# Performance work log

Measured on AMD Instinct MI355X. Metric: run time of the kernel, lower is better.

## Reference

```python
import math
import jax, jax.numpy as jnp
import numpy as np

EPS = 1e-5
KS = 8          # emb_ks == emb_hs
NH = 4          # attention heads
LOOKBACK = 5
NLAYERS = 4


def prelu(x, a):
    return jnp.where(x >= 0, x, a * x)


def ln_c(x, g, b):
    # LayerNormalization4D: stats over channel dim; note (std + eps) denominator
    mu = jnp.mean(x, 1, keepdims=True)
    var = jnp.mean((x - mu) ** 2, 1, keepdims=True)
    return (x - mu) / (jnp.sqrt(var + EPS) + EPS) * g[None, :, None, None] + b[None, :, None, None]


def ln_cf_head(x, g, b):
    # x: [H, B, E, T, F]; stats over (E, F); g, b: [H, E, F]
    mu = jnp.mean(x, (2, 4), keepdims=True)
    var = jnp.mean((x - mu) ** 2, (2, 4), keepdims=True)
    return (x - mu) / (jnp.sqrt(var + EPS) + EPS) * g[:, None, :, None, :] + b[:, None, :, None, :]


def ln_cf_proj(x, g, b):
    # x: [B, C, T, F]; stats over (C, F); g, b: [C, F]
    mu = jnp.mean(x, (1, 3), keepdims=True)
    var = jnp.mean((x - mu) ** 2, (1, 3), keepdims=True)
    return (x - mu) / (jnp.sqrt(var + EPS) + EPS) * g[None, :, None, :] + b[None, :, None, :]


def lstm(x, wih, whh, bih, bhh):
    # x: [N, T, I] -> hidden sequence [N, T, H]; PyTorch gate order i, f, g, o
    xp = jnp.einsum('nti,gi->ntg', x, wih) + bih + bhh
    H = whh.shape[1]
    N = x.shape[0]

    def step(carry, xt):
        h, c = carry
        gates = xt + h @ whh.T
        i, f, g, o = jnp.split(gates, 4, axis=-1)
        c = jax.nn.sigmoid(f) * c + jax.nn.sigmoid(i) * jnp.tanh(g)
        h = jax.nn.sigmoid(o) * jnp.tanh(c)
        return (h, c), h

    init = (jnp.zeros((N, H), x.dtype), jnp.zeros((N, H), x.dtype))
    _, hs = jax.lax.scan(step, init, jnp.swapaxes(xp, 0, 1))
    return jnp.swapaxes(hs, 0, 1)


def bilstm(x, wih, whh, bih, bhh):
    fwd = lstm(x, wih[0], whh[0], bih[0], bhh[0])
    bwd = lstm(x[:, ::-1], wih[1], whh[1], bih[1], bhh[1])[:, ::-1]
    return jnp.concatenate([fwd, bwd], -1)


def unfold1d(x):
    # non-overlapping unfold (ks == stride == KS): [N, C, L] -> [N, L//KS, C*KS]
    N, C, Lx = x.shape
    return x.reshape(N, C, Lx // KS, KS).transpose(0, 2, 1, 3).reshape(N, Lx // KS, C * KS)


def fold1d(h, w, b):
    # ConvTranspose1d with stride == kernel == KS; h: [N, Lp, D], w: [D, C, KS]
    y = jnp.einsum('nld,dck->nlck', h, w)
    N, Lp, C, K = y.shape
    return y.transpose(0, 2, 1, 3).reshape(N, C, Lp * K) + b[None, :, None]


def conv2d(x, w, b):
    y = jax.lax.conv_general_dilated(x, w, (1, 1), ((1, 1), (1, 1)),
                                     dimension_numbers=('NCHW', 'OIHW', 'NCHW'))
    return y + b[None, :, None, None]


def block(x, p):
    B, C, oT, oF = x.shape
    T = math.ceil((oT - KS) / KS) * KS + KS
    F = math.ceil((oF - KS) / KS) * KS + KS
    x = jnp.pad(x, ((0, 0), (0, 0), (0, T - oT), (0, F - oF)))
    input_ = x
    # intra (frequency) bidirectional LSTM
    z = ln_c(input_, p['intra_norm_g'], p['intra_norm_b'])
    z = z.transpose(0, 2, 1, 3).reshape(B * T, C, F)
    z = unfold1d(z)                                    # [B*T, F//KS, C*KS]
    h = bilstm(z, p['intra_wih'], p['intra_whh'], p['intra_bih'], p['intra_bhh'])
    z = fold1d(h, p['intra_lin_w'], p['intra_lin_b'])  # [B*T, C, F]
    intra = z.reshape(B, T, C, F).transpose(0, 2, 1, 3) + input_
    # inter (time) causal LSTM
    z = ln_c(intra, p['inter_norm_g'], p['inter_norm_b'])
    z = z.transpose(0, 3, 1, 2).reshape(B * F, C, T)
    z = unfold1d(z)                                    # [B*F, T//KS, C*KS]
    h = lstm(z, p['inter_wih'], p['inter_whh'], p['inter_bih'], p['inter_bhh'])
    z = fold1d(h, p['inter_lin_w'], p['inter_lin_b'])  # [B*F, C, T]
    inter = z.reshape(B, F, C, T).transpose(0, 2, 3, 1) + intra
    inter = inter[..., :oT, :oF]

    # per-head 1x1-conv QKV (batched over heads) + local causal attention
    def qkv(w, b, a, g, beta):
        y = jnp.einsum('bctf,hec->hbetf', inter, w) + b[:, None, :, None, None]
        y = prelu(y, a[:, None, None, None, None])
        return ln_cf_head(y, g, beta)

    Q = qkv(p['q_w'], p['q_b'], p['q_a'], p['q_g'], p['q_beta'])
    K = qkv(p['k_w'], p['k_b'], p['k_a'], p['k_g'], p['k_beta'])
    V = qkv(p['v_w'], p['v_b'], p['v_a'], p['v_g'], p['v_beta'])
    E = Q.shape[2]
    CV = V.shape[2]
    Qf = Q.transpose(0, 1, 3, 2, 4).reshape(NH, B, oT, E * oF)
    Kf = K.transpose(0, 1, 3, 2, 4).reshape(NH, B, oT, E * oF)
    Vf = V.transpose(0, 1, 3, 2, 4).reshape(NH, B, oT, CV * oF)
    attn = jnp.einsum('hbtd,hbsd->hbts', Qf, Kf) / jnp.sqrt(jnp.asarray(E * oF, Qf.dtype))
    t = jnp.arange(oT)
    d = t[:, None] - t[None, :]
    mask = (d >= 0) & (d <= LOOKBACK)      # causal with 5-frame lookback
    attn = jnp.where(mask, attn, -1e30)
    A = jax.nn.softmax(attn, axis=-1)
    O = jnp.einsum('hbts,hbsd->hbtd', A, Vf).reshape(NH, B, oT, CV, oF)
    O = O.transpose(1, 0, 3, 2, 4).reshape(B, NH * CV, oT, oF)
    y = jnp.einsum('bctf,dc->bdtf', O, p['proj_w']) + p['proj_b'][None, :, None, None]
    y = prelu(y, p['proj_a'])
    y = ln_cf_proj(y, p['proj_g'], p['proj_beta'])
    return y + inter


def _forward(x, conv_w, conv_b, gn_g, gn_b,
             intra_norm_g, intra_norm_b, intra_wih, intra_whh, intra_bih, intra_bhh,
             intra_lin_w, intra_lin_b,
             inter_norm_g, inter_norm_b, inter_wih, inter_whh, inter_bih, inter_bhh,
             inter_lin_w, inter_lin_b,
             q_w, q_b, q_a, q_g, q_beta,
             k_w, k_b, k_a, k_g, k_beta,
             v_w, v_b, v_a, v_g, v_beta,
             proj_w, proj_b, proj_a, proj_g, proj_beta,
             deconv_w, deconv_b):
    esti = conv2d(x, conv_w, conv_b)
    # GroupNorm(1, emb_dim): per-sample stats over (C, T, F), per-channel affine
    mu = jnp.mean(esti, (1, 2, 3), keepdims=True)
    var = jnp.mean((esti - mu) ** 2, (1, 2, 3), keepdims=True)
    esti = (esti - mu) / jnp.sqrt(var + EPS) * gn_g[None, :, None, None] + gn_b[None, :, None, None]
    stacked = dict(
        intra_norm_g=intra_norm_g, intra_norm_b=intra_norm_b,
        intra_wih=intra_wih, intra_whh=intra_whh, intra_bih=intra_bih, intra_bhh=intra_bhh,
        intra_lin_w=intra_lin_w, intra_lin_b=intra_lin_b,
        inter_norm_g=inter_norm_g, inter_norm_b=inter_norm_b,
        inter_wih=inter_wih, inter_whh=inter_whh, inter_bih=inter_bih, inter_bhh=inter_bhh,
        inter_lin_w=inter_lin_w, inter_lin_b=inter_lin_b,
        q_w=q_w, q_b=q_b, q_a=q_a, q_g=q_g, q_beta=q_beta,
        k_w=k_w, k_b=k_b, k_a=k_a, k_g=k_g, k_beta=k_beta,
        v_w=v_w, v_b=v_b, v_a=v_a, v_g=v_g, v_beta=v_beta,
        proj_w=proj_w, proj_b=proj_b, proj_a=proj_a, proj_g=proj_g, proj_beta=proj_beta,
    )
    for l in range(NLAYERS):
        p = {k: v[l] for k, v in stacked.items()}
        esti = block(esti, p)
    # ConvTranspose2d(k=3, s=1, p=1) == conv with spatially flipped, io-swapped kernel, pad 1
    w2 = jnp.flip(deconv_w, (2, 3)).transpose(1, 0, 2, 3)
    return conv2d(esti, w2, deconv_b)


def setup_inputs() -> dict:
    key = jax.random.key(0)
    keys = iter(jax.random.split(key, 80))

    def rn(shape, s=0.05):
        return jax.random.normal(next(keys), shape, jnp.float32) * s

    L, C, H, E, CV, FA = 4, 32, 256, 4, 8, 161
    IN = C * KS
    return dict(
        x=jax.random.normal(next(keys), (8, 2, 504, 161), jnp.float32),
        conv_w=rn((C, 2, 3, 3)), conv_b=jnp.zeros((C,), jnp.float32),
        gn_g=jnp.ones((C,), jnp.float32), gn_b=jnp.zeros((C,), jnp.float32),
        intra_norm_g=jnp.ones((L, C), jnp.float32), intra_norm_b=jnp.zeros((L, C), jnp.float32),
        intra_wih=rn((L, 2, 4 * H, IN)), intra_whh=rn((L, 2, 4 * H, H)),
        intra_bih=jnp.zeros((L, 2, 4 * H), jnp.float32), intra_bhh=jnp.zeros((L, 2, 4 * H), jnp.float32),
        intra_lin_w=rn((L, 2 * H, C, KS)), intra_lin_b=jnp.zeros((L, C), jnp.float32),
        inter_norm_g=jnp.ones((L, C), jnp.float32), inter_norm_b=jnp.zeros((L, C), jnp.float32),
        inter_wih=rn((L, 4 * H, IN)), inter_whh=rn((L, 4 * H, H)),
        inter_bih=jnp.zeros((L, 4 * H), jnp.float32), inter_bhh=jnp.zeros((L, 4 * H), jnp.float32),
        inter_lin_w=rn((L, H, C, KS)), inter_lin_b=jnp.zeros((L, C), jnp.float32),
        q_w=rn((L, NH, E, C)), q_b=jnp.zeros((L, NH, E), jnp.float32),
        q_a=jnp.full((L, NH), 0.25, jnp.float32),
        q_g=jnp.ones((L, NH, E, FA), jnp.float32), q_beta=jnp.zeros((L, NH, E, FA), jnp.float32),
        k_w=rn((L, NH, E, C)), k_b=jnp.zeros((L, NH, E), jnp.float32),
        k_a=jnp.full((L, NH), 0.25, jnp.float32),
        k_g=jnp.ones((L, NH, E, FA), jnp.float32), k_beta=jnp.zeros((L, NH, E, FA), jnp.float32),
        v_w=rn((L, NH, CV, C)), v_b=jnp.zeros((L, NH, CV), jnp.float32),
        v_a=jnp.full((L, NH), 0.25, jnp.float32),
        v_g=jnp.ones((L, NH, CV, FA), jnp.float32), v_beta=jnp.zeros((L, NH, CV, FA), jnp.float32),
        proj_w=rn((L, C, C)), proj_b=jnp.zeros((L, C), jnp.float32),
        proj_a=jnp.full((L,), 0.25, jnp.float32),
        proj_g=jnp.ones((L, C, FA), jnp.float32), proj_beta=jnp.zeros((L, C, FA), jnp.float32),
        deconv_w=rn((C, 2, 3, 3)), deconv_b=jnp.zeros((2,), jnp.float32),
    )


def reference(x, conv_w, conv_b, gn_g, gn_b,
              intra_norm_g, intra_norm_b, intra_wih, intra_whh, intra_bih, intra_bhh,
              intra_lin_w, intra_lin_b,
              inter_norm_g, inter_norm_b, inter_wih, inter_whh, inter_bih, inter_bhh,
              inter_lin_w, inter_lin_b,
              q_w, q_b, q_a, q_g, q_beta,
              k_w, k_b, k_a, k_g, k_beta,
              v_w, v_b, v_a, v_g, v_beta,
              proj_w, proj_b, proj_a, proj_g, proj_beta,
              deconv_w, deconv_b):
    return _forward(x, conv_w, conv_b, gn_g, gn_b,
                    intra_norm_g, intra_norm_b, intra_wih, intra_whh, intra_bih, intra_bhh,
                    intra_lin_w, intra_lin_b,
                    inter_norm_g, inter_norm_b, inter_wih, inter_whh, inter_bih, inter_bhh,
                    inter_lin_w, inter_lin_b,
                    q_w, q_b, q_a, q_g, q_beta,
                    k_w, k_b, k_a, k_g, k_beta,
                    v_w, v_b, v_a, v_g, v_beta,
                    proj_w, proj_b, proj_a, proj_g, proj_beta,
                    deconv_w, deconv_b)
```

## Files before the change

### kernel.cpp

```cpp
#include <hip/hip_runtime.h>
#include <hip/hip_bf16.h>
#include <math.h>

#define BB   8
#define CH   32
#define TT   504
#define FFp  168
#define OF   161
#define KSZ  8
#define HID  256
#define NG   1024
#define NHh  4
#define EE   4
#define CVv  8
#define N1   4032
#define N2   1344
#define LFi  21
#define LTi  63
#define EPSf 1e-5f

#define AS1 __attribute__((address_space(1)))
#define AS3 __attribute__((address_space(3)))

typedef __hip_bfloat16 bf16;
// ... 69 lines not shown
          int ff = f + kw - 1;
          xv[ci][kh][kw] = (ff < 0) ? 0.f : xs[(ci * 3 + kh) * (OF + 3) + ff];
        }
    for (int co = 0; co < CH; co++) {
      float acc = bias[co];
#pragma unroll
      for (int ci = 0; ci < 2; ci++)
#pragma unroll
        for (int kh = 0; kh < 3; kh++)
#pragma unroll
          for (int kw = 0; kw < 3; kw++)
            acc += xv[ci][kh][kw] * w[((co * 2 + ci) * 3 + kh) * 3 + kw];
      out[((size_t)(b * CH + co) * TT + t) * OF + f] = f2b(acc);
    }
  }
}

__global__ __launch_bounds__(256) void gn_reduce_k(const bf16* __restrict__ xin,
                                                   float* __restrict__ stats) {
  const int M = CH * TT * OF;
  int b = blockIdx.x >> 6;
  int part = blockIdx.x & 63;
  const bf16* p = xin + (size_t)b * M;
  float s1 = 0.f, s2 = 0.f;
  for (int i = part * 256 + threadIdx.x; i < M; i += 64 * 256) {
    float v = b2f(p[i]);
    s1 += v; s2 += v * v;
  }
  __shared__ float red[8];
  block_reduce2(s1, s2, red);
  if (threadIdx.x == 0) {
    atomicAdd(&stats[b * 2], s1);
    atomicAdd(&stats[b * 2 + 1], s2);
  }
}

__global__ __launch_bounds__(256) void gn_apply_k(const bf16* __restrict__ xin,
                                                  const float* __restrict__ stats,
                                                  const float* __restrict__ g,
                                                  const float* __restrict__ bb,
                                                  bf16* __restrict__ act) {
  int gid = blockIdx.x * 256 + threadIdx.x;
  int f = gid % FFp;
  int t = (gid / FFp) % TT;
  int c = (gid / (FFp * TT)) % CH;
  int b = gid / (FFp * TT * CH);
  float v = 0.f;
  if (f < OF) {
    const float M = (float)(CH * TT * OF);
    float mu = stats[b * 2] / M;
    float var = stats[b * 2 + 1] / M - mu * mu;
    float xv = b2f(xin[((size_t)(b * CH + c) * TT + t) * OF + f]);
    v = (xv - mu) * rsqrtf(var + EPSf) * g[c] + bb[c];
  }
  act[gid] = f2b(v);
}

__global__ __launch_bounds__(256) void ln_unfold_k(const bf16* __restrict__ xin,
                                                   const float* __restrict__ g,
                                                   const float* __restrict__ bb,
                                                   bf16* __restrict__ out) {
  __shared__ float sm[CH * FFp];
  __shared__ float mu_s[FFp], rs_s[FFp];
  __shared__ float gg[CH], bv[CH];
  int bt = blockIdx.x;
  int b = bt / TT, t = bt % TT;
  int tid = threadIdx.x;
  if (tid < CH) { gg[tid] = g[tid]; bv[tid] = bb[tid]; }
  const short* base = (const short*)xin + ((size_t)b * CH * TT + t) * FFp;
  for (int idx = tid; idx < CH * LFi; idx += 256) {
    int c = idx / LFi, ck = idx % LFi;
    int f0 = ck * 8;
    s16x8 v = *(const s16x8*)(base + (size_t)c * TT * FFp + f0);
#pragma unroll
    for (int k = 0; k < 8; k++) sm[c * FFp + f0 + k] = us2f((unsigned short)v[k]);
  }
  __syncthreads();
  if (tid < FFp) {
    int f = tid;
    float s1 = 0.f, s2 = 0.f;
#pragma unroll
    for (int c = 0; c < CH; c++) { float v = sm[c * FFp + f]; s1 += v; s2 += v * v; }
    float mu = s1 / CH;
    float var = s2 / CH - mu * mu;
    mu_s[f] = mu;
    rs_s[f] = 1.f / (sqrtf(var + EPSf) + EPSf);
  }
  __syncthreads();
  unsigned short* outu = (unsigned short*)out;
  for (int ch = tid; ch < LFi * CH; ch += 256) {
    int gI = ch >> 5, c = ch & 31;
    float gc = gg[c], bc = bv[c];
    unsigned short o8[8];
#pragma unroll
    for (int k = 0; k < 8; k++) {
      int f = gI * 8 + k;
      float v = (sm[c * FFp + f] - mu_s[f]) * rs_s[f] * gc + bc;
      o8[k] = f2bu(v);
    }
    *(uint4*)(outu + ((size_t)gI * N1 + bt) * 256 + c * 8) = *(uint4*)o8;
  }
}

__global__ __launch_bounds__(256) void ln_unfold8_k(const bf16* __restrict__ xin,
                                                    const float* __restrict__ g,
                                                    const float* __restrict__ bb,
                                                    bf16* __restrict__ out) {
  __shared__ short smb[8 * CH * FFp];
  __shared__ float mu_s[8 * FFp], rs_s[8 * FFp];
  __shared__ float gg[CH], bv[CH];
  int tg = blockIdx.x, b = blockIdx.y;
  int tid = threadIdx.x;
  if (tid < CH) { gg[tid] = g[tid]; bv[tid] = bb[tid]; }
  const short* src = (const short*)xin;
  for (int idx = tid; idx < 8 * CH * (FFp / 8); idx += 256) {
    int t8 = idx / (CH * 21);
    int rem = idx % (CH * 21);
    int c = rem / 21, fc = rem % 21;
    s16x8 v = *(const s16x8*)(src + ((size_t)(b * CH + c) * TT + tg * 8 + t8) * FFp + fc * 8);
    *(s16x8*)(&smb[(t8 * CH + c) * FFp + fc * 8]) = v;
  }
  __syncthreads();
  for (int p = tid; p < 8 * FFp; p += 256) {
    int t8 = p / FFp, f = p % FFp;
    float s1 = 0.f, s2 = 0.f;
#pragma unroll
    for (int c = 0; c < CH; c++) {
      float v = us2f((unsigned short)smb[(t8 * CH + c) * FFp + f]);
      s1 += v; s2 += v * v;
    }
    float mu = s1 / CH;
    float var = s2 / CH - mu * mu;
    mu_s[p] = mu;
    rs_s[p] = 1.f / (sqrtf(var + EPSf) + EPSf);
  }
  __syncthreads();
  unsigned short* outu = (unsigned short*)out;
  for (int ch = tid; ch < FFp * CH; ch += 256) {
    int f = ch >> 5, c = ch & 31;
    float gc = gg[c], bc = bv[c];
    unsigned short o8[8];
#pragma unroll
    for (int k = 0; k < 8; k++) {
      float v = us2f((unsigned short)smb[(k * CH + c) * FFp + f]);
      v = (v - mu_s[k * FFp + f]) * rs_s[k * FFp + f] * gc + bc;
      o8[k] = f2bu(v);
    }
    *(uint4*)(outu + ((size_t)tg * N2 + b * FFp + f) * 256 + c * 8) = *(uint4*)o8;
  }
}

__global__ __launch_bounds__(256) void lstm_prep_k(const float* __restrict__ wih0,
                                                   const float* __restrict__ whh0,
                                                   bf16* __restrict__ blob0) {
  int dir = blockIdx.y;
  const float* wih = wih0 + (size_t)dir * 262144;
  const float* whh = whh0 + (size_t)dir * 262144;
  unsigned short* blob = (unsigned short*)(blob0 + (size_t)dir * 524288);
  int gid = blockIdx.x * 256 + threadIdx.x;
  int lane = gid & 63;
  int ks = (gid >> 6) & 15;
  int nt = gid >> 10;
  int n = nt * 16 + (lane & 15);
  int kb = ks * 32 + (lane >> 4) * 8;
  unsigned short o8[8];
#pragma unroll
  for (int j = 0; j < 8; j++) {
    int k = kb + j;
    float v = (k < 256) ? wih[n * 256 + k] : whh[n * 256 + (k - 256)];
    o8[j] = f2bu(v);
  }
  *(uint4*)(blob + (size_t)gid * 8) = *(uint4*)o8;
}

template<int PH>
__device__ __forceinline__ void lstm_run(short* __restrict__ afr,
                                         short* __restrict__ bst_w,
                                         const short* __restrict__ xzs,
                                         const short* __restrict__ blob,
                                         const float* __restrict__ bih,
                                         const float* __restrict__ bhh,
                                         unsigned short* __restrict__ houtu,
                                         int N, int Ls, int hstride, int hoff,
                                         int n0, int dirrev, int w, int lane) {
  int tid = w * 64 + lane;
  int l15 = lane & 15, lq = lane >> 4;

  float bias[4][2];
#pragma unroll
  for (int q = 0; q < 4; q++)
#pragma unroll
    for (int j = 0; j < 2; j++) {
      int n = q * 256 + (2 * w + j) * 16 + l15;
      bias[q][j] = bih[n] + bhh[n];
    }
  for (int i = tid; i < 8192; i += 512) afr[8192 + i] = 0;
  float cst[16];
#pragma unroll
  for (int i = 0; i < 16; i++) cst[i] = 0.f;

#define BQ_ISSUE(P)                                                              \
  {                                                                              \
    const int a_ = (((P) >> 4) + PH) & 3;                                        \
    const int r_ = ((P) >> 1) & 7, h2_ = (P) & 1;                                \
    const int nt_ = (r_ >> 1) * 16 + 2 * w + (r_ & 1);                           \
    const short* gb_ = blob + (size_t)nt_ * 8192 + (a_ * 4 + h2_ * 2) * 512 + lane * 8; \
    short* lb_ = bst_w + ((P) % 6) * 1024;                                       \
    _Pragma("unroll")                                                            \
    for (int k_ = 0; k_ < 2; k_++)                                               \
      __builtin_amdgcn_global_load_lds((const AS1 void*)(gb_ + k_ * 512),        \
                                       (AS3 void*)(lb_ + k_ * 512), 16, 0, 0);   \
  }

  for (int st = 0; st < Ls; st++) {
    int t = dirrev ? (Ls - 1 - st) : st;
    {
      const short* gx = xzs + ((size_t)t * N + n0 + l15) * 256 + (w * 4 + lq) * 8;
      __builtin_amdgcn_global_load_lds((const AS1 void*)gx,
                                       (AS3 void*)(afr + (w * 2 + 0) * 512), 16, 0, 2);
      __builtin_amdgcn_global_load_lds((const AS1 void*)(gx + 16 * 256),
                                       (AS3 void*)(afr + (w * 2 + 1) * 512), 16, 0, 2);
    }
    BQ_ISSUE(0);
    BQ_ISSUE(1);
    BQ_ISSUE(2);
    BQ_ISSUE(3);
    BQ_ISSUE(4);
    __syncthreads();

    f32x4 acc[2][4][2];
#pragma unroll
    for (int mt = 0; mt < 2; mt++)
#pragma unroll
      for (int q = 0; q < 4; q++)
#pragma unroll
        for (int j = 0; j < 2; j++)
          acc[mt][q][j] = (f32x4){bias[q][j], bias[q][j], bias[q][j], bias[q][j]};

    s16x8 af[4][2];
#pragma unroll
    for (int C = 0; C < 64; C++) {
      const int s = C >> 1, h2 = C & 1;
      const int rR = s & 7;
      const int q = rR >> 1, j = rR & 1;
      if (rR == 0 && h2 == 0) {
        const int a = ((s >> 3) + PH) & 3;
#pragma unroll
        for (int k = 0; k < 4; k++)
#pragma unroll
          for (int mt = 0; mt < 2; mt++)
            af[k][mt] = *(const s16x8*)(&afr[(((a * 4 + k) * 2 + mt) * 64 + lane) * 8]);
      }
      if (C <= 59)      __builtin_amdgcn_s_waitcnt(0x0F78);
      else if (C == 60) __builtin_amdgcn_s_waitcnt(0x0F76);
      else if (C == 61) __builtin_amdgcn_s_waitcnt(0x0F74);
      else if (C == 62) __builtin_amdgcn_s_waitcnt(0x0F72);
      else              __builtin_amdgcn_s_waitcnt(0x0F70);
      const short* lb = bst_w + (C % 6) * 1024;
#pragma unroll
      for (int k = 0; k < 2; k++) {
        s16x8 bf = *(const s16x8*)(lb + k * 512 + lane * 8);
        acc[0][q][j] = __builtin_amdgcn_mfma_f32_16x16x32_bf16(af[h2 * 2 + k][0], bf, acc[0][q][j], 0, 0, 0);
        acc[1][q][j] = __builtin_amdgcn_mfma_f32_16x16x32_bf16(af[h2 * 2 + k][1], bf, acc[1][q][j], 0, 0, 0);
      }
      if (C < 59) BQ_ISSUE(C + 5);
    }
    __syncthreads();

#pragma unroll
    for (int mt = 0; mt < 2; mt++)
#pragma unroll
      for (int j = 0; j < 2; j++) {
        int d = (2 * w + j) * 16 + l15;
        int slotb = ((8 + (d >> 5)) * 2 + mt) * 64 + ((d >> 3) & 3) * 16;
#pragma unroll
        for (int r = 0; r < 4; r++) {
          int m = lq * 4 + r;
          float iv = sigm(acc[mt][0][j][r]);
          float fv = sigm(acc[mt][1][j][r]);
          float gv = tanh_f(acc[mt][2][j][r]);
          float ov = sigm(acc[mt][3][j][r]);
          float c = fv * cst[mt * 8 + j * 4 + r] + iv * gv;
          cst[mt * 8 + j * 4 + r] = c;
          float h = ov * tanh_f(c);
          unsigned short hb = f2bu(h);
          houtu[((size_t)t * N + n0 + mt * 16 + m) * hstride + hoff + d] = hb;
          afr[(slotb + m) * 8 + (d & 7)] = (short)hb;
        }
      }
  }
#undef BQ_ISSUE
}

__global__ __launch_bounds__(512) void lstm_mfma_k(const bf16* __restrict__ xz,
                                                   const bf16* __restrict__ blob0,
                                                   const float* __restrict__ bih0,
                                                   const float* __restrict__ bhh0,
                                                   bf16* __restrict__ hout,
                                                   int N, int Ls, int hstride, int bidir) {
  __shared__ __attribute__((aligned(16))) short afr[16 * 2 * 64 * 8];
  __shared__ __attribute__((aligned(16))) short bstage[8 * 6 * 1024];
  int tid = threadIdx.x;
  int w = tid >> 6, lane = tid & 63;
  int dir = blockIdx.y;
  const short* blob = (const short*)(blob0 + (size_t)dir * 524288);
  const float* bih = bih0 + dir * NG;
  const float* bhh = bhh0 + dir * NG;
  int hoff = dir * 256;
  int n0 = blockIdx.x * 32;
  int dirrev = (bidir && dir) ? 1 : 0;
  unsigned short* houtu = (unsigned short*)hout;
  const short* xzs = (const short*)xz;
  short* bst_w = bstage + w * 6144;
  int PH = ((blockIdx.x >> 3) + blockIdx.x) & 3;
  switch (PH) {
    case 0: lstm_run<0>(afr, bst_w, xzs, blob, bih, bhh, houtu, N, Ls, hstride, hoff, n0, dirrev, w, lane); break;
    case 1: lstm_run<1>(afr, bst_w, xzs, blob, bih, bhh, houtu, N, Ls, hstride, hoff, n0, dirrev, w, lane); break;
    case 2: lstm_run<2>(afr, bst_w, xzs, blob, bih, bhh, houtu, N, Ls, hstride, hoff, n0, dirrev, w, lane); break;
    default: lstm_run<3>(afr, bst_w, xzs, blob, bih, bhh, houtu, N, Ls, hstride, hoff, n0, dirrev, w, lane); break;
  }
}

__global__ __launch_bounds__(256) void fold_gemm_k(const bf16* __restrict__ A,
                                                   const float* __restrict__ Bw,
                                                   const float* __restrict__ linb,
                                                   const bf16* __restrict__ resid,
                                                   bf16* __restrict__ outp,
                                                   int K, int mode) {
  __shared__ float As[16 * 68];
  __shared__ float Bs[16 * 64];
  int tid = threadIdx.x;
  int n0 = blockIdx.x * 64;
  int m0 = blockIdx.y * 64;
  int tr = tid >> 4, tc = tid & 15;
  float acc[4][4] = {};
  int arow = tid >> 2, akg = (tid & 3) * 4;
  int bkk = tid >> 4, bc4 = (tid & 15) * 4;
  for (int k0 = 0; k0 < K; k0 += 16) {
    ushort4 avu = *(const ushort4*)((const unsigned short*)A + (size_t)(m0 + arow) * K + k0 + akg);
    float4 bv = *(const float4*)(Bw + (size_t)(k0 + bkk) * 256 + n0 + bc4);
    __syncthreads();
    As[(akg + 0) * 68 + arow] = us2f(avu.x);
    As[(akg + 1) * 68 + arow] = us2f(avu.y);
    As[(akg + 2) * 68 + arow] = us2f(avu.z);
    As[(akg + 3) * 68 + arow] = us2f(avu.w);
    *(float4*)(&Bs[bkk * 64 + bc4]) = bv;
    __syncthreads();
#pragma unroll
    for (int kk = 0; kk < 16; kk++) {
      float4 a4 = *(const float4*)(&As[kk * 68 + tr * 4]);
      float4 b4 = *(const float4*)(&Bs[kk * 64 + tc * 4]);
      float aa[4] = {a4.x, a4.y, a4.z, a4.w};
      float bb_[4] = {b4.x, b4.y, b4.z, b4.w};
#pragma unroll
      for (int i = 0; i < 4; i++)
#pragma unroll
        for (int j = 0; j < 4; j++) acc[i][j] += aa[i] * bb_[j];
    }
  }
#pragma unroll
  for (int i = 0; i < 4; i++) {
    int r = m0 + tr * 4 + i;
#pragma unroll
    for (int j = 0; j < 4; j++) {
      int col = n0 + tc * 4 + j;
      int c = col >> 3, kp = col & 7;
      float v = acc[i][j] + linb[c];
      if (mode == 0) {
        int l = r / N1, n = r % N1;
        int b = n / TT, t = n % TT;
        size_t o = ((size_t)(b * CH + c) * TT + t) * FFp + (l * 8 + kp);
        outp[o] = f2b(v + b2f(resid[o]));
      } else {
        int l = r / N2, n = r % N2;
        int b = n / FFp, fq = n % FFp;
        int t = l * 8 + kp;
        if (fq < OF) {
          size_t o = ((size_t)(b * CH + c) * TT + t) * OF + fq;
          size_t ri = ((size_t)(b * CH + c) * TT + t) * FFp + fq;
          outp[o] = f2b(v + b2f(resid[ri]));
        }
      }
    }
  }
}

__global__ __launch_bounds__(256) void qkv_k(const bf16* __restrict__ interc,
    const float* __restrict__ qw, const float* __restrict__ qb, const float* __restrict__ qa,
    const float* __restrict__ qg, const float* __restrict__ qbeta,
    const float* __restrict__ kw, const float* __restrict__ kb, const float* __restrict__ ka,
    const float* __restrict__ kg, const float* __restrict__ kbeta,
    const float* __restrict__ vw, const float* __restrict__ vb, const float* __restrict__ va,
    const float* __restrict__ vg, const float* __restrict__ vbeta,
    bf16* __restrict__ qo, bf16* __restrict__ ko, bf16* __restrict__ vo) {
  __shared__ float sm[CH * OF];
  __shared__ float wb[16 * 32];
  __shared__ float wbias[16];
  __shared__ float yb[16 * OF];
  __shared__ float red[8];
  int bt = blockIdx.x, h = blockIdx.y;
  int b = bt / TT, t = bt % TT;
  int tid = threadIdx.x;
  const short* src = (const short*)interc + ((size_t)b * CH * TT + t) * OF;
  for (int idx = tid; idx < CH * 21; idx += 256) {
    int c = idx / 21, ck = idx % 21;
    if (ck < 20) {
      int f0 = ck * 8;
      s16x8 v = ld8u(src + (size_t)c * TT * OF + f0);
#pragma unroll
      for (int k = 0; k < 8; k++) sm[c * OF + f0 + k] = us2f((unsigned short)v[k]);
    } else {
      sm[c * OF + 160] = us2f((unsigned short)src[(size_t)c * TT * OF + 160]);
    }
  }
  for (int idx = tid; idx < 512; idx += 256) {
    int e = idx >> 5, c = idx & 31;
    float w;
    if (e < 4) w = qw[(h * 4 + e) * 32 + c];
    else if (e < 8) w = kw[(h * 4 + e - 4) * 32 + c];
    else w = vw[(h * 8 + e - 8) * 32 + c];
    wb[idx] = w;
  }
  if (tid < 16) {
    float bv;
    if (tid < 4) bv = qb[h * 4 + tid];
    else if (tid < 8) bv = kb[h * 4 + tid - 4];
    else bv = vb[h * 8 + tid - 8];
    wbias[tid] = bv;
  }
  __syncthreads();
  float aQ = qa[h], aK = ka[h], aV = va[h];
  for (int idx = tid; idx < 16 * OF; idx += 256) {
    int e = idx / OF, f = idx % OF;
    float accv = wbias[e];
#pragma unroll
    for (int c = 0; c < 32; c++) accv += sm[c * OF + f] * wb[e * 32 + c];
    float a = e < 4 ? aQ : (e < 8 ? aK : aV);
    yb[idx] = accv >= 0.f ? accv : a * accv;
  }
  __syncthreads();
  for (int seg = 0; seg < 3; seg++) {
    int s0 = (seg == 0) ? 0 : ((seg == 1) ? 644 : 1288);
    int len = (seg == 2) ? 1288 : 644;
    float s1 = 0.f, s2 = 0.f;
    for (int i = tid; i < len; i += 256) { float v = yb[s0 + i]; s1 += v; s2 += v * v; }
    block_reduce2(s1, s2, red);
    float mu = s1 / len;
    float var = s2 / len - mu * mu;
    float rs = 1.f / (sqrtf(var + EPSf) + EPSf);
    const float* gp; const float* bp; bf16* op; int nch;
    if (seg == 0) { gp = qg; bp = qbeta; op = qo; nch = 4; }
    else if (seg == 1) { gp = kg; bp = kbeta; op = ko; nch = 4; }
    else { gp = vg; bp = vbeta; op = vo; nch = 8; }
    for (int i = tid; i < len; i += 256) {
      int e = i / OF, f = i % OF;
      float v = (yb[s0 + i] - mu) * rs * gp[(h * nch + e) * OF + f] + bp[(h * nch + e) * OF + f];
      op[(((size_t)(h * BB + b) * nch + e) * TT + t) * OF + f] = f2b(v);
    }
  }
}

__global__ __launch_bounds__(256) void attn_k(const bf16* __restrict__ Q,
                                              const bf16* __restrict__ Kt,
                                              const bf16* __restrict__ V,
                                              bf16* __restrict__ O) {
  int t = blockIdx.x;
  int hb = blockIdx.y;
  int h = hb >> 3, b = hb & 7;
  int tid = threadIdx.x;
  int nv = min(t, 5) + 1;
  const float scale = 0.0394055201f;
  __shared__ float redl[24];
// ... 97 lines not shown
  int b = bt / TT, t = bt % TT;
  int tid = threadIdx.x;
  const short* src = (const short*)ob + ((size_t)b * CH * TT + t) * OF;
  for (int idx = tid; idx < CH * 21; idx += 256) {
    int c = idx / 21, ck = idx % 21;
    if (ck < 20) {
      int f0 = ck * 8;
      s16x8 v = ld8u(src + (size_t)c * TT * OF + f0);
#pragma unroll
      for (int k = 0; k < 8; k++) sm[c * OF + f0 + k] = us2f((unsigned short)v[k]);
    } else {
      sm[c * OF + 160] = us2f((unsigned short)src[(size_t)c * TT * OF + 160]);
    }
  }
  for (int idx = tid; idx < CH * CH; idx += 256) wsm[idx] = pw[idx];
  __syncthreads();
  float aP = pa[0];
  for (int idx = tid; idx < CH * OF; idx += 256) {
    int d = idx / OF, f = idx % OF;
    float accv = pb[d];
#pragma unroll
    for (int c = 0; c < 32; c++) accv += sm[c * OF + f] * wsm[d * 32 + c];
    yb[idx] = accv >= 0.f ? accv : aP * accv;
  }
  __syncthreads();
  float s1 = 0.f, s2 = 0.f;
  for (int i = tid; i < CH * OF; i += 256) { float v = yb[i]; s1 += v; s2 += v * v; }
  block_reduce2(s1, s2, red);
  const float Mn = (float)(CH * OF);
  float mu = s1 / Mn;
  float var = s2 / Mn - mu * mu;
  float rs = 1.f / (sqrtf(var + EPSf) + EPSf);
  for (int idx = tid; idx < CH * FFp; idx += 256) {
    int d = idx / FFp, f = idx % FFp;
    float v = 0.f;
    if (f < OF) {
      float y = (yb[d * OF + f] - mu) * rs * pg[d * OF + f] + pbeta[d * OF + f];
      v = y + b2f(interc[((size_t)(b * CH + d) * TT + t) * OF + f]);
    }
    act[((size_t)(b * CH + d) * TT + t) * FFp + f] = f2b(v);
  }
}

__global__ __launch_bounds__(256) void deconv_k(const bf16* __restrict__ act,
                                                const float* __restrict__ w,
                                                const float* __restrict__ bias,
                                                float* __restrict__ out) {
  __shared__ float ash[CH * 3 * FFp];
  int bt = blockIdx.x;
  int b = bt / TT, t = bt % TT;
  int tid = threadIdx.x;
  const short* acts = (const short*)act;
  for (int ch = tid; ch < CH * 3 * (FFp / 8); ch += 256) {
    int ci = ch / 63, rem = ch % 63;
    int rr = rem / 21, fc = rem % 21;
    int ts = t + rr - 1;
    float* dst = &ash[(ci * 3 + rr) * FFp + fc * 8];
    if (ts < 0 || ts >= TT) {
#pragma unroll
      for (int k2 = 0; k2 < 8; k2++) dst[k2] = 0.f;
    } else {
      s16x8 v = *(const s16x8*)(acts + ((size_t)(b * CH + ci) * TT + ts) * FFp + fc * 8);
#pragma unroll
      for (int k2 = 0; k2 < 8; k2++) dst[k2] = us2f((unsigned short)v[k2]);
    }
  }
  __syncthreads();
  int f = tid;
  if (f < OF) {
    float acc0 = bias[0], acc1 = bias[1];
#pragma unroll 4
    for (int ci = 0; ci < CH; ci++) {
      const float* row = &ash[ci * 3 * FFp];
      float xv[3][3];
#pragma unroll
      for (int kh = 0; kh < 3; kh++)
#pragma unroll
        for (int kw = 0; kw < 3; kw++) {
          int ff = f + kw - 1;
          xv[kh][kw] = (ff < 0) ? 0.f : row[kh * FFp + ff];
        }
#pragma unroll
      for (int kh = 0; kh < 3; kh++)
#pragma unroll
        for (int kw = 0; kw < 3; kw++) {
          acc0 += xv[kh][kw] * w[((ci * 2 + 0) * 3 + (2 - kh)) * 3 + (2 - kw)];
          acc1 += xv[kh][kw] * w[((ci * 2 + 1) * 3 + (2 - kh)) * 3 + (2 - kw)];
        }
    }
    out[((size_t)(b * 2 + 0) * TT + t) * OF + f] = acc0;
    out[((size_t)(b * 2 + 1) * TT + t) * OF + f] = acc1;
  }
}

extern "C" void kernel_launch(void* const* d_in, const int* in_sizes, int n_in,
                              void* d_out, int out_size, void* d_ws, size_t ws_size,
                              hipStream_t stream) {
  const float* x            = (const float*)d_in[0];
  const float* conv_w       = (const float*)d_in[1];
  const float* conv_b       = (const float*)d_in[2];
  const float* gn_g         = (const float*)d_in[3];
  const float* gn_b         = (const float*)d_in[4];
  const float* intra_norm_g = (const float*)d_in[5];
  const float* intra_norm_b = (const float*)d_in[6];
  const float* intra_wih    = (const float*)d_in[7];
  const float* intra_whh    = (const float*)d_in[8];
  const float* intra_bih    = (const float*)d_in[9];
  const float* intra_bhh    = (const float*)d_in[10];
  const float* intra_lin_w  = (const float*)d_in[11];
  const float* intra_lin_b  = (const float*)d_in[12];
  const float* inter_norm_g = (const float*)d_in[13];
  const float* inter_norm_b = (const float*)d_in[14];
  const float* inter_wih    = (const float*)d_in[15];
  const float* inter_whh    = (const float*)d_in[16];
  const float* inter_bih    = (const float*)d_in[17];
  const float* inter_bhh    = (const float*)d_in[18];
  const float* inter_lin_w  = (const float*)d_in[19];
  const float* inter_lin_b  = (const float*)d_in[20];
  const float* q_w    = (const float*)d_in[21];
  const float* q_b    = (const float*)d_in[22];
  const float* q_a    = (const float*)d_in[23];
  const float* q_g    = (const float*)d_in[24];
  const float* q_beta = (const float*)d_in[25];
  const float* k_w    = (const float*)d_in[26];
  const float* k_b    = (const float*)d_in[27];
  const float* k_a    = (const float*)d_in[28];
  const float* k_g    = (const float*)d_in[29];
  const float* k_beta = (const float*)d_in[30];
  const float* v_w    = (const float*)d_in[31];
  const float* v_b    = (const float*)d_in[32];
  const float* v_a    = (const float*)d_in[33];
  const float* v_g    = (const float*)d_in[34];
  const float* v_beta = (const float*)d_in[35];
  const float* proj_w    = (const float*)d_in[36];
  const float* proj_b    = (const float*)d_in[37];
  const float* proj_a    = (const float*)d_in[38];
  const float* proj_g    = (const float*)d_in[39];
  const float* proj_beta = (const float*)d_in[40];
  const float* deconv_w  = (const float*)d_in[41];
  const float* deconv_b  = (const float*)d_in[42];

  float* stats = (float*)d_ws;
  bf16* arena  = (bf16*)((char*)d_ws + 256);
  bf16* act    = arena;
  bf16* tmp    = arena + 21676032;
  bf16* hbuf   = arena + 43352064;
  bf16* res    = arena + 86704128;
  bf16* interc = arena + 108380160;
  bf16* convout = interc;
  bf16* qbuf = act;
  bf16* kbuf = tmp;
  bf16* vbuf = res;
  bf16* obuf = hbuf;
  bf16* blob_intra = res;
  bf16* blob_inter = interc;

  hipMemsetAsync(stats, 0, 64 * sizeof(float), stream);
  conv_in_k<<<4032, 192, 0, stream>>>(x, conv_w, conv_b, convout);
  gn_reduce_k<<<512, 256, 0, stream>>>(convout, stats);
  gn_apply_k<<<84672, 256, 0, stream>>>(convout, stats, gn_g, gn_b, act);

  for (int l = 0; l < 4; l++) {
    lstm_prep_k<<<dim3(256, 2), 256, 0, stream>>>(
        intra_wih + (size_t)l * 524288, intra_whh + (size_t)l * 524288, blob_intra);
    ln_unfold_k<<<4032, 256, 0, stream>>>(act, intra_norm_g + l * 32, intra_norm_b + l * 32, tmp);
    lstm_mfma_k<<<dim3(126, 2), 512, 0, stream>>>(
        tmp, blob_intra, intra_bih + l * 2048, intra_bhh + l * 2048, hbuf, N1, LFi, 512, 1);
    fold_gemm_k<<<dim3(4, 1323), 256, 0, stream>>>(
        hbuf, intra_lin_w + (size_t)l * 131072, intra_lin_b + l * 32, act, res, 512, 0);
    lstm_prep_k<<<dim3(256, 1), 256, 0, stream>>>(
        inter_wih + (size_t)l * 262144, inter_whh + (size_t)l * 262144, blob_inter);
    ln_unfold8_k<<<dim3(LTi, BB), 256, 0, stream>>>(res, inter_norm_g + l * 32, inter_norm_b + l * 32, tmp);
    lstm_mfma_k<<<dim3(42, 1), 512, 0, stream>>>(
        tmp, blob_inter, inter_bih + l * 1024, inter_bhh + l * 1024, hbuf, N2, LTi, 256, 0);
    fold_gemm_k<<<dim3(4, 1323), 256, 0, stream>>>(
        hbuf, inter_lin_w + (size_t)l * 65536, inter_lin_b + l * 32, res, interc, 256, 1);
    qkv_k<<<dim3(4032, 4), 256, 0, stream>>>(interc,
        q_w + l * 512, q_b + l * 16, q_a + l * 4, q_g + l * 2576, q_beta + l * 2576,
        k_w + l * 512, k_b + l * 16, k_a + l * 4, k_g + l * 2576, k_beta + l * 2576,
        v_w + l * 1024, v_b + l * 32, v_a + l * 4, v_g + l * 5152, v_beta + l * 5152,
        qbuf, kbuf, vbuf);
    attn_k<<<dim3(504, 32), 256, 0, stream>>>(qbuf, kbuf, vbuf, obuf);
    proj_k<<<4032, 256, 0, stream>>>(obuf, proj_w + l * 1024, proj_b + l * 32, proj_a + l,
                                     proj_g + l * 5152, proj_beta + l * 5152, interc, act);
  }
  deconv_k<<<4032, 256, 0, stream>>>(act, deconv_w, deconv_b, (float*)d_out);
}
```

Measured before the change: 14.86 ms.

## Quantize LSTM weights to int8 with per-row scales and dequantize in-register

LSTM weight preparation now quantizes the stacked input and recurrent weights to int8 with one scale per gate row, which halves the bytes streamed from global memory into LDS on every timestep. The MFMA loop widens its prefetch to eleven in-flight chunks over a twelve-slot staging ring and turns each int8 chunk back into bf16 with shifts and a scale multiply before the MFMAs. This adds ALU work to the latency-bound recurrent inner loop and loses weight precision compared with bf16, so outputs can drift from the reference.

```diff
diff --git a/kernel.cpp b/kernel.cpp
--- a/kernel.cpp
+++ b/kernel.cpp
@@ -245,32 +245,55 @@
 
 __global__ __launch_bounds__(256) void lstm_prep_k(const float* __restrict__ wih0,
                                                    const float* __restrict__ whh0,
-                                                   bf16* __restrict__ blob0) {
+                                                   unsigned char* __restrict__ blob0) {
   int dir = blockIdx.y;
   const float* wih = wih0 + (size_t)dir * 262144;
   const float* whh = whh0 + (size_t)dir * 262144;
-  unsigned short* blob = (unsigned short*)(blob0 + (size_t)dir * 524288);
-  int gid = blockIdx.x * 256 + threadIdx.x;
-  int lane = gid & 63;
-  int ks = (gid >> 6) & 15;
-  int nt = gid >> 10;
-  int n = nt * 16 + (lane & 15);
-  int kb = ks * 32 + (lane >> 4) * 8;
-  unsigned short o8[8];
-#pragma unroll
-  for (int j = 0; j < 8; j++) {
-    int k = kb + j;
-    float v = (k < 256) ? wih[n * 256 + k] : whh[n * 256 + (k - 256)];
-    o8[j] = f2bu(v);
-  }
-  *(uint4*)(blob + (size_t)gid * 8) = *(uint4*)o8;
+  unsigned char* blob = blob0 + (size_t)dir * 1048576;
+  float* scales = (float*)(blob + 524288);
+  int wv = threadIdx.x >> 6, lane = threadIdx.x & 63;
+  for (int rr = 0; rr < 16; rr++) {
+    int n = (blockIdx.x * 4 + wv) * 16 + rr;
+    float4 a = *(const float4*)(wih + (size_t)n * 256 + lane * 4);
+    float4 bq = *(const float4*)(whh + (size_t)n * 256 + lane * 4);
+    float m = fmaxf(fmaxf(fabsf(a.x), fabsf(a.y)), fmaxf(fabsf(a.z), fabsf(a.w)));
+    m = fmaxf(m, fmaxf(fmaxf(fabsf(bq.x), fabsf(bq.y)), fmaxf(fabsf(bq.z), fabsf(bq.w))));
+#pragma unroll
+    for (int off = 32; off > 0; off >>= 1) m = fmaxf(m, __shfl_xor(m, off, 64));
+    float inv = (m > 0.f) ? 127.f / m : 0.f;
+    if (lane == 0) scales[n] = (m > 0.f) ? m / 127.f : 1.f;
+    int nt = n >> 4, l15 = n & 15;
+    {
+      int k0 = lane * 4;
+      int kf = k0 >> 5, lq = (k0 >> 3) & 3, jb = k0 & 7;
+      int kfp = kf >> 1, half = kf & 1;
+      float v[4] = {a.x, a.y, a.z, a.w};
+      unsigned char q4[4];
+#pragma unroll
+      for (int i = 0; i < 4; i++) q4[i] = (unsigned char)(signed char)(int)rintf(v[i] * inv);
+      size_t addr = (((size_t)nt * 8 + kfp) * 64 + (lq * 16 + l15)) * 16 + half * 8 + jb;
+      *(unsigned int*)(blob + addr) = *(unsigned int*)q4;
+    }
+    {
+      int k0 = 256 + lane * 4;
+      int kf = k0 >> 5, lq = (k0 >> 3) & 3, jb = k0 & 7;
+      int kfp = kf >> 1, half = kf & 1;
+      float v[4] = {bq.x, bq.y, bq.z, bq.w};
+      unsigned char q4[4];
+#pragma unroll
+      for (int i = 0; i < 4; i++) q4[i] = (unsigned char)(signed char)(int)rintf(v[i] * inv);
+      size_t addr = (((size_t)nt * 8 + kfp) * 64 + (lq * 16 + l15)) * 16 + half * 8 + jb;
+      *(unsigned int*)(blob + addr) = *(unsigned int*)q4;
+    }
+  }
 }
 
 template<int PH>
 __device__ __forceinline__ void lstm_run(short* __restrict__ afr,
                                          short* __restrict__ bst_w,
                                          const short* __restrict__ xzs,
-                                         const short* __restrict__ blob,
+                                         const unsigned char* __restrict__ blob8,
+                                         const float* __restrict__ scales,
                                          const float* __restrict__ bih,
                                          const float* __restrict__ bhh,
                                          unsigned short* __restrict__ houtu,
@@ -280,12 +303,14 @@
   int l15 = lane & 15, lq = lane >> 4;
 
   float bias[4][2];
+  float sc[4][2];
 #pragma unroll
   for (int q = 0; q < 4; q++)
 #pragma unroll
     for (int j = 0; j < 2; j++) {
       int n = q * 256 + (2 * w + j) * 16 + l15;
       bias[q][j] = bih[n] + bhh[n];
+      sc[q][j] = scales[n];
     }
   for (int i = tid; i < 8192; i += 512) afr[8192 + i] = 0;
   float cst[16];
@@ -297,12 +322,9 @@
     const int a_ = (((P) >> 4) + PH) & 3;                                        \
     const int r_ = ((P) >> 1) & 7, h2_ = (P) & 1;                                \
     const int nt_ = (r_ >> 1) * 16 + 2 * w + (r_ & 1);                           \
-    const short* gb_ = blob + (size_t)nt_ * 8192 + (a_ * 4 + h2_ * 2) * 512 + lane * 8; \
-    short* lb_ = bst_w + ((P) % 6) * 1024;                                       \
-    _Pragma("unroll")                                                            \
-    for (int k_ = 0; k_ < 2; k_++)                                               \
-      __builtin_amdgcn_global_load_lds((const AS1 void*)(gb_ + k_ * 512),        \
-                                       (AS3 void*)(lb_ + k_ * 512), 16, 0, 0);   \
+    const unsigned char* gb_ = blob8 + (((size_t)nt_ * 8 + a_ * 2 + h2_) * 64 + lane) * 16; \
+    __builtin_amdgcn_global_load_lds((const AS1 void*)gb_,                       \
+                                     (AS3 void*)(bst_w + ((P) % 12) * 512), 16, 0, 0); \
   }
 
   for (int st = 0; st < Ls; st++) {
@@ -314,11 +336,9 @@
       __builtin_amdgcn_global_load_lds((const AS1 void*)(gx + 16 * 256),
                                        (AS3 void*)(afr + (w * 2 + 1) * 512), 16, 0, 2);
     }
-    BQ_ISSUE(0);
-    BQ_ISSUE(1);
-    BQ_ISSUE(2);
-    BQ_ISSUE(3);
-    BQ_ISSUE(4);
+    BQ_ISSUE(0);  BQ_ISSUE(1);  BQ_ISSUE(2);  BQ_ISSUE(3);
+    BQ_ISSUE(4);  BQ_ISSUE(5);  BQ_ISSUE(6);  BQ_ISSUE(7);
+    BQ_ISSUE(8);  BQ_ISSUE(9);  BQ_ISSUE(10);
     __syncthreads();
 
     f32x4 acc[2][4][2];
@@ -344,19 +364,35 @@
           for (int mt = 0; mt < 2; mt++)
             af[k][mt] = *(const s16x8*)(&afr[(((a * 4 + k) * 2 + mt) * 64 + lane) * 8]);
       }
-      if (C <= 59)      __builtin_amdgcn_s_waitcnt(0x0F78);
-      else if (C == 60) __builtin_amdgcn_s_waitcnt(0x0F76);
-      else if (C == 61) __builtin_amdgcn_s_waitcnt(0x0F74);
-      else if (C == 62) __builtin_amdgcn_s_waitcnt(0x0F72);
+      if (C <= 53)      __builtin_amdgcn_s_waitcnt(0x0F7A);
+      else if (C == 54) __builtin_amdgcn_s_waitcnt(0x0F79);
+      else if (C == 55) __builtin_amdgcn_s_waitcnt(0x0F78);
+      else if (C == 56) __builtin_amdgcn_s_waitcnt(0x0F77);
+      else if (C == 57) __builtin_amdgcn_s_waitcnt(0x0F76);
+      else if (C == 58) __builtin_amdgcn_s_waitcnt(0x0F75);
+      else if (C == 59) __builtin_amdgcn_s_waitcnt(0x0F74);
+      else if (C == 60) __builtin_amdgcn_s_waitcnt(0x0F73);
+      else if (C == 61) __builtin_amdgcn_s_waitcnt(0x0F72);
+      else if (C == 62) __builtin_amdgcn_s_waitcnt(0x0F71);
       else              __builtin_amdgcn_s_waitcnt(0x0F70);
-      const short* lb = bst_w + (C % 6) * 1024;
+      const short* lb = bst_w + (C % 12) * 512;
+      s16x8 raw = *(const s16x8*)(lb + lane * 8);
+      union { s16x8 v; unsigned int uw[4]; } u;
+      u.v = raw;
+      float scv = sc[q][j];
 #pragma unroll
       for (int k = 0; k < 2; k++) {
-        s16x8 bf = *(const s16x8*)(lb + k * 512 + lane * 8);
+        s16x8 bf;
+#pragma unroll
+        for (int jj = 0; jj < 8; jj++) {
+          int word = (int)u.uw[k * 2 + (jj >> 2)];
+          int val = (word << (24 - 8 * (jj & 3))) >> 24;
+          bf[jj] = (short)f2bu((float)val * scv);
+        }
         acc[0][q][j] = __builtin_amdgcn_mfma_f32_16x16x32_bf16(af[h2 * 2 + k][0], bf, acc[0][q][j], 0, 0, 0);
         acc[1][q][j] = __builtin_amdgcn_mfma_f32_16x16x32_bf16(af[h2 * 2 + k][1], bf, acc[1][q][j], 0, 0, 0);
       }
-      if (C < 59) BQ_ISSUE(C + 5);
+      if (C < 53) BQ_ISSUE(C + 11);
     }
     __syncthreads();
 
@@ -386,17 +422,18 @@
 }
 
 __global__ __launch_bounds__(512) void lstm_mfma_k(const bf16* __restrict__ xz,
-                                                   const bf16* __restrict__ blob0,
+                                                   const unsigned char* __restrict__ blob0,
                                                    const float* __restrict__ bih0,
                                                    const float* __restrict__ bhh0,
                                                    bf16* __restrict__ hout,
                                                    int N, int Ls, int hstride, int bidir) {
   __shared__ __attribute__((aligned(16))) short afr[16 * 2 * 64 * 8];
-  __shared__ __attribute__((aligned(16))) short bstage[8 * 6 * 1024];
+  __shared__ __attribute__((aligned(16))) short bstage[8 * 12 * 512];
   int tid = threadIdx.x;
   int w = tid >> 6, lane = tid & 63;
   int dir = blockIdx.y;
-  const short* blob = (const short*)(blob0 + (size_t)dir * 524288);
+  const unsigned char* blob8 = blob0 + (size_t)dir * 1048576;
+  const float* scales = (const float*)(blob8 + 524288);
   const float* bih = bih0 + dir * NG;
   const float* bhh = bhh0 + dir * NG;
   int hoff = dir * 256;
@@ -407,10 +444,10 @@
   short* bst_w = bstage + w * 6144;
   int PH = ((blockIdx.x >> 3) + blockIdx.x) & 3;
   switch (PH) {
-    case 0: lstm_run<0>(afr, bst_w, xzs, blob, bih, bhh, houtu, N, Ls, hstride, hoff, n0, dirrev, w, lane); break;
-    case 1: lstm_run<1>(afr, bst_w, xzs, blob, bih, bhh, houtu, N, Ls, hstride, hoff, n0, dirrev, w, lane); break;
-    case 2: lstm_run<2>(afr, bst_w, xzs, blob, bih, bhh, houtu, N, Ls, hstride, hoff, n0, dirrev, w, lane); break;
-    default: lstm_run<3>(afr, bst_w, xzs, blob, bih, bhh, houtu, N, Ls, hstride, hoff, n0, dirrev, w, lane); break;
+    case 0: lstm_run<0>(afr, bst_w, xzs, blob8, scales, bih, bhh, houtu, N, Ls, hstride, hoff, n0, dirrev, w, lane); break;
+    case 1: lstm_run<1>(afr, bst_w, xzs, blob8, scales, bih, bhh, houtu, N, Ls, hstride, hoff, n0, dirrev, w, lane); break;
+    case 2: lstm_run<2>(afr, bst_w, xzs, blob8, scales, bih, bhh, houtu, N, Ls, hstride, hoff, n0, dirrev, w, lane); break;
+    default: lstm_run<3>(afr, bst_w, xzs, blob8, scales, bih, bhh, houtu, N, Ls, hstride, hoff, n0, dirrev, w, lane); break;
   }
 }
 
@@ -814,8 +851,8 @@
   bf16* kbuf = tmp;
   bf16* vbuf = res;
   bf16* obuf = hbuf;
-  bf16* blob_intra = res;
-  bf16* blob_inter = interc;
+  unsigned char* blob_intra = (unsigned char*)res;
+  unsigned char* blob_inter = (unsigned char*)interc;
 
   hipMemsetAsync(stats, 0, 64 * sizeof(float), stream);
   conv_in_k<<<4032, 192, 0, stream>>>(x, conv_w, conv_b, convout);
@@ -823,14 +860,14 @@
   gn_apply_k<<<84672, 256, 0, stream>>>(convout, stats, gn_g, gn_b, act);
 
   for (int l = 0; l < 4; l++) {
-    lstm_prep_k<<<dim3(256, 2), 256, 0, stream>>>(
+    lstm_prep_k<<<dim3(16, 2), 256, 0, stream>>>(
         intra_wih + (size_t)l * 524288, intra_whh + (size_t)l * 524288, blob_intra);
     ln_unfold_k<<<4032, 256, 0, stream>>>(act, intra_norm_g + l * 32, intra_norm_b + l * 32, tmp);
     lstm_mfma_k<<<dim3(126, 2), 512, 0, stream>>>(
         tmp, blob_intra, intra_bih + l * 2048, intra_bhh + l * 2048, hbuf, N1, LFi, 512, 1);
     fold_gemm_k<<<dim3(4, 1323), 256, 0, stream>>>(
         hbuf, intra_lin_w + (size_t)l * 131072, intra_lin_b + l * 32, act, res, 512, 0);
-    lstm_prep_k<<<dim3(256, 1), 256, 0, stream>>>(
+    lstm_prep_k<<<dim3(16, 1), 256, 0, stream>>>(
         inter_wih + (size_t)l * 262144, inter_whh + (size_t)l * 262144, blob_inter);
     ln_unfold8_k<<<dim3(LTi, BB), 256, 0, stream>>>(res, inter_norm_g + l * 32, inter_norm_b + l * 32, tmp);
     lstm_mfma_k<<<dim3(42, 1), 512, 0, stream>>>(
```

New measurement: 15.10 ms. Within noise of the previous version (+1.6%).

## Process 64 sequences per LSTM block to reuse recurrent weight tiles

Applied to the files above, without the earlier changes.

The MFMA LSTM kernel now handles 64 rows per workgroup instead of 32, so each staged weight tile feeds four M-tiles instead of two. This halves the number of blocks that stream the full recurrent and input weight blob every timestep. The loop order is changed so the A fragments are loaded per k-half, and the weight staging ring drops from 6 slots to 5 with a prefetch distance of 4 to fit the larger LDS A buffer. The trade-off is fewer blocks (63x2 and 21), which lowers parallelism on a GPU with many CUs, plus higher register and LDS pressure.

```diff
diff --git a/kernel.cpp b/kernel.cpp
--- a/kernel.cpp
+++ b/kernel.cpp
@@ -287,18 +287,18 @@
       int n = q * 256 + (2 * w + j) * 16 + l15;
       bias[q][j] = bih[n] + bhh[n];
     }
-  for (int i = tid; i < 8192; i += 512) afr[8192 + i] = 0;
-  float cst[16];
-#pragma unroll
-  for (int i = 0; i < 16; i++) cst[i] = 0.f;
+  for (int i = tid; i < 16384; i += 512) afr[16384 + i] = 0;
+  float cst[32];
+#pragma unroll
+  for (int i = 0; i < 32; i++) cst[i] = 0.f;
 
 #define BQ_ISSUE(P)                                                              \
   {                                                                              \
     const int a_ = (((P) >> 4) + PH) & 3;                                        \
-    const int r_ = ((P) >> 1) & 7, h2_ = (P) & 1;                                \
+    const int h2_ = ((P) >> 3) & 1, r_ = (P) & 7;                                \
     const int nt_ = (r_ >> 1) * 16 + 2 * w + (r_ & 1);                           \
     const short* gb_ = blob + (size_t)nt_ * 8192 + (a_ * 4 + h2_ * 2) * 512 + lane * 8; \
-    short* lb_ = bst_w + ((P) % 6) * 1024;                                       \
+    short* lb_ = bst_w + ((P) % 5) * 1024;                                       \
     _Pragma("unroll")                                                            \
     for (int k_ = 0; k_ < 2; k_++)                                               \
       __builtin_amdgcn_global_load_lds((const AS1 void*)(gb_ + k_ * 512),        \
@@ -307,65 +307,63 @@
 
   for (int st = 0; st < Ls; st++) {
     int t = dirrev ? (Ls - 1 - st) : st;
-    {
-      const short* gx = xzs + ((size_t)t * N + n0 + l15) * 256 + (w * 4 + lq) * 8;
+#pragma unroll
+    for (int mt = 0; mt < 4; mt++) {
+      const short* gx = xzs + ((size_t)t * N + n0 + mt * 16 + l15) * 256 + (w * 4 + lq) * 8;
       __builtin_amdgcn_global_load_lds((const AS1 void*)gx,
-                                       (AS3 void*)(afr + (w * 2 + 0) * 512), 16, 0, 2);
-      __builtin_amdgcn_global_load_lds((const AS1 void*)(gx + 16 * 256),
-                                       (AS3 void*)(afr + (w * 2 + 1) * 512), 16, 0, 2);
+                                       (AS3 void*)(afr + (w * 4 + mt) * 512), 16, 0, 2);
     }
     BQ_ISSUE(0);
     BQ_ISSUE(1);
     BQ_ISSUE(2);
     BQ_ISSUE(3);
-    BQ_ISSUE(4);
     __syncthreads();
 
-    f32x4 acc[2][4][2];
-#pragma unroll
-    for (int mt = 0; mt < 2; mt++)
+    f32x4 acc[4][4][2];
+#pragma unroll
+    for (int mt = 0; mt < 4; mt++)
 #pragma unroll
       for (int q = 0; q < 4; q++)
 #pragma unroll
         for (int j = 0; j < 2; j++)
           acc[mt][q][j] = (f32x4){bias[q][j], bias[q][j], bias[q][j], bias[q][j]};
 
-    s16x8 af[4][2];
+    s16x8 af[2][4];
 #pragma unroll
     for (int C = 0; C < 64; C++) {
-      const int s = C >> 1, h2 = C & 1;
-      const int rR = s & 7;
-      const int q = rR >> 1, j = rR & 1;
-      if (rR == 0 && h2 == 0) {
-        const int a = ((s >> 3) + PH) & 3;
-#pragma unroll
-        for (int k = 0; k < 4; k++)
-#pragma unroll
-          for (int mt = 0; mt < 2; mt++)
-            af[k][mt] = *(const s16x8*)(&afr[(((a * 4 + k) * 2 + mt) * 64 + lane) * 8]);
+      const int a = ((C >> 4) + PH) & 3;
+      const int h2 = (C >> 3) & 1;
+      const int r = C & 7;
+      const int q = r >> 1, j = r & 1;
+      if (r == 0) {
+#pragma unroll
+        for (int k = 0; k < 2; k++)
+#pragma unroll
+          for (int mt = 0; mt < 4; mt++)
+            af[k][mt] = *(const s16x8*)(&afr[(((a * 4 + h2 * 2 + k) * 4 + mt) * 64 + lane) * 8]);
       }
-      if (C <= 59)      __builtin_amdgcn_s_waitcnt(0x0F78);
-      else if (C == 60) __builtin_amdgcn_s_waitcnt(0x0F76);
+      if (C <= 60)      __builtin_amdgcn_s_waitcnt(0x0F76);
       else if (C == 61) __builtin_amdgcn_s_waitcnt(0x0F74);
       else if (C == 62) __builtin_amdgcn_s_waitcnt(0x0F72);
       else              __builtin_amdgcn_s_waitcnt(0x0F70);
-      const short* lb = bst_w + (C % 6) * 1024;
+      const short* lb = bst_w + (C % 5) * 1024;
 #pragma unroll
       for (int k = 0; k < 2; k++) {
         s16x8 bf = *(const s16x8*)(lb + k * 512 + lane * 8);
-        acc[0][q][j] = __builtin_amdgcn_mfma_f32_16x16x32_bf16(af[h2 * 2 + k][0], bf, acc[0][q][j], 0, 0, 0);
-        acc[1][q][j] = __builtin_amdgcn_mfma_f32_16x16x32_bf16(af[h2 * 2 + k][1], bf, acc[1][q][j], 0, 0, 0);
+#pragma unroll
+        for (int mt = 0; mt < 4; mt++)
+          acc[mt][q][j] = __builtin_amdgcn_mfma_f32_16x16x32_bf16(af[k][mt], bf, acc[mt][q][j], 0, 0, 0);
       }
-      if (C < 59) BQ_ISSUE(C + 5);
+      if (C < 60) BQ_ISSUE(C + 4);
     }
     __syncthreads();
 
 #pragma unroll
-    for (int mt = 0; mt < 2; mt++)
+    for (int mt = 0; mt < 4; mt++)
 #pragma unroll
       for (int j = 0; j < 2; j++) {
         int d = (2 * w + j) * 16 + l15;
-        int slotb = ((8 + (d >> 5)) * 2 + mt) * 64 + ((d >> 3) & 3) * 16;
+        int slotb = ((8 + (d >> 5)) * 4 + mt) * 64 + ((d >> 3) & 3) * 16;
 #pragma unroll
         for (int r = 0; r < 4; r++) {
           int m = lq * 4 + r;
@@ -391,8 +389,8 @@
                                                    const float* __restrict__ bhh0,
                                                    bf16* __restrict__ hout,
                                                    int N, int Ls, int hstride, int bidir) {
-  __shared__ __attribute__((aligned(16))) short afr[16 * 2 * 64 * 8];
-  __shared__ __attribute__((aligned(16))) short bstage[8 * 6 * 1024];
+  __shared__ __attribute__((aligned(16))) short afr[16 * 4 * 64 * 8];
+  __shared__ __attribute__((aligned(16))) short bstage[8 * 5 * 1024];
   int tid = threadIdx.x;
   int w = tid >> 6, lane = tid & 63;
   int dir = blockIdx.y;
@@ -400,11 +398,11 @@
   const float* bih = bih0 + dir * NG;
   const float* bhh = bhh0 + dir * NG;
   int hoff = dir * 256;
-  int n0 = blockIdx.x * 32;
+  int n0 = blockIdx.x * 64;
   int dirrev = (bidir && dir) ? 1 : 0;
   unsigned short* houtu = (unsigned short*)hout;
   const short* xzs = (const short*)xz;
-  short* bst_w = bstage + w * 6144;
+  short* bst_w = bstage + w * 5120;
   int PH = ((blockIdx.x >> 3) + blockIdx.x) & 3;
   switch (PH) {
     case 0: lstm_run<0>(afr, bst_w, xzs, blob, bih, bhh, houtu, N, Ls, hstride, hoff, n0, dirrev, w, lane); break;
@@ -826,14 +824,14 @@
     lstm_prep_k<<<dim3(256, 2), 256, 0, stream>>>(
         intra_wih + (size_t)l * 524288, intra_whh + (size_t)l * 524288, blob_intra);
     ln_unfold_k<<<4032, 256, 0, stream>>>(act, intra_norm_g + l * 32, intra_norm_b + l * 32, tmp);
-    lstm_mfma_k<<<dim3(126, 2), 512, 0, stream>>>(
+    lstm_mfma_k<<<dim3(63, 2), 512, 0, stream>>>(
         tmp, blob_intra, intra_bih + l * 2048, intra_bhh + l * 2048, hbuf, N1, LFi, 512, 1);
     fold_gemm_k<<<dim3(4, 1323), 256, 0, stream>>>(
         hbuf, intra_lin_w + (size_t)l * 131072, intra_lin_b + l * 32, act, res, 512, 0);
     lstm_prep_k<<<dim3(256, 1), 256, 0, stream>>>(
         inter_wih + (size_t)l * 262144, inter_whh + (size_t)l * 262144, blob_inter);
     ln_unfold8_k<<<dim3(LTi, BB), 256, 0, stream>>>(res, inter_norm_g + l * 32, inter_norm_b + l * 32, tmp);
-    lstm_mfma_k<<<dim3(42, 1), 512, 0, stream>>>(
+    lstm_mfma_k<<<dim3(21, 1), 512, 0, stream>>>(
         tmp, blob_inter, inter_bih + l * 1024, inter_bhh + l * 1024, hbuf, N2, LTi, 256, 0);
     fold_gemm_k<<<dim3(4, 1323), 256, 0, stream>>>(
         hbuf, inter_lin_w + (size_t)l * 65536, inter_lin_b + l * 32, res, interc, 256, 1);
```

Result: slower. 20.00 ms (+34.6%).
